# Optimization experiments

Hardware: AMD Instinct MI355X
Metric: run time of the kernel (lower is better)

## Reference

```python
import jax, jax.numpy as jnp
import numpy as np

B, S, D = 2, 2048, 2560
H, HD = 32, 80           # n_head, head_dim = n_embd // n_head
RD = 32                  # rotary_dim (partial rotary, phi-style)
ROPE_BASE = 10000.0


def _rope_cache(seqlen, rotary_dim):
    # inv_freq = 1 / base^(2i/d); freqs = outer(t, inv_freq)  -> [S, RD//2]
    inv_freq = 1.0 / (ROPE_BASE ** (jnp.arange(0, rotary_dim, 2, dtype=jnp.float32) / rotary_dim))
    t = jnp.arange(seqlen, dtype=jnp.float32)
    freqs = jnp.outer(t, inv_freq)
    return jnp.cos(freqs), jnp.sin(freqs)


def setup_inputs() -> dict:
    key = jax.random.key(0)
    k0, k1, k2, k3, k4 = jax.random.split(key, 5)
    x = jax.random.normal(k0, (B, S, D), dtype=jnp.float32)
    wqkv_w = jax.random.normal(k1, (3 * D, D), dtype=jnp.float32) * 0.02
    wqkv_b = jax.random.normal(k2, (3 * D,), dtype=jnp.float32) * 0.02
    out_w = jax.random.normal(k3, (D, D), dtype=jnp.float32) * 0.02
    out_b = jax.random.normal(k4, (D,), dtype=jnp.float32) * 0.02
    return {"x": x, "wqkv_w": wqkv_w, "wqkv_b": wqkv_b, "out_w": out_w, "out_b": out_b}


def _attention_core(x, wqkv_w, wqkv_b, out_w, out_b):
    b, s, d = x.shape
    qkv = (x @ wqkv_w.T + wqkv_b).reshape(b, s, 3, H, HD)  # [B,S,3,H,HD]

    cos, sin = _rope_cache(s, RD)            # [S, RD//2]
    c = cos[:, None, :]                       # [S,1,RD//2]
    si = sin[:, None, :]

    def rot(t):  # partial NeoX-style rotary on first RD dims; t: [B,S,H,HD]
        t_rot, t_pass = t[..., :RD], t[..., RD:]
        t1, t2 = t_rot[..., : RD // 2], t_rot[..., RD // 2 :]
        return jnp.concatenate([t1 * c - t2 * si, t1 * si + t2 * c, t_pass], axis=-1)

    q = rot(qkv[:, :, 0])                     # [B,S,H,HD]
    k = rot(qkv[:, :, 1])
    v = qkv[:, :, 2]

    # fp32 scores = q @ (k * scale)^T, causal mask filled with -10000.0 (as in source)
    scale = 1.0 / np.sqrt(HD).astype(np.float32)
    scores = jnp.einsum("bqhd,bkhd->bhqk", q, k * scale)  # [B,H,S,S]
    causal_mask = jnp.arange(s)[None, :] > jnp.arange(s)[:, None]  # cols > rows
    scores = jnp.where(causal_mask, jnp.float32(-10000.0), scores)
    attn = jax.nn.softmax(scores, axis=-1)
    ctx = jnp.einsum("bhqk,bkhd->bqhd", attn, v).reshape(b, s, d)
    return ctx @ out_w.T + out_b


def reference(x, wqkv_w, wqkv_b, out_w, out_b):
    return _attention_core(x, wqkv_w, wqkv_b, out_w, out_b)
```

## Files before the change

### kernel.cpp

```cpp
#include <hip/hip_runtime.h>
#include <cstdint>
#include <cstddef>

#define B_  2
#define S_  2048
#define D_  2560
#define H_  32
#define HD_ 80

typedef __attribute__((ext_vector_type(8))) short  short8;
typedef __attribute__((ext_vector_type(4))) float  floatx4;

__device__ __forceinline__ float b2f(unsigned short u) {
  union { unsigned int i; float f; } x; x.i = ((unsigned int)u) << 16; return x.f;
}
__device__ __forceinline__ unsigned short f2bf(float f) {
  union { float f; unsigned int i; } x; x.f = f;
  unsigned int u = x.i;
  return (unsigned short)((u + 0x7fffu + ((u >> 16) & 1u)) >> 16);
}

__global__ void cvt3_kernel(const float* __restrict__ s0, unsigned short* __restrict__ d0, int n0,
                            const float* __restrict__ s1, unsigned short* __restrict__ d1, int n1,
                            const float* __restrict__ s2, unsigned short* __restrict__ d2, int n2) {
  int j = blockIdx.x * 256 + threadIdx.x;
  const float* s; unsigned short* d;
  if (j < n0) { s = s0; d = d0; }
  else {
    j -= n0;
    if (j < n1) { s = s1; d = d1; }
    else { j -= n1; if (j >= n2) return; s = s2; d = d2; }
  }
  const float4 v = ((const float4*)s)[j];
  ushort4 r;
  r.x = f2bf(v.x); r.y = f2bf(v.y); r.z = f2bf(v.z); r.w = f2bf(v.w);
  ((ushort4*)d)[j] = r;
}

#define GLOAD_LDS16(g, l)                                                      \
  __builtin_amdgcn_global_load_lds(                                            \
      (const __attribute__((address_space(1))) void*)(g),                      \
      (__attribute__((address_space(3))) void*)(l), 16, 0, 0)

template <int OUT_BF16, int MSUB, int NSUB>
__global__ __launch_bounds__(512)
void gemm256(const unsigned short* __restrict__ A,
             const unsigned short* __restrict__ Bw,
             const float* __restrict__ bias,
             void* __restrict__ Cv,
             const int M, const int N, const int K) {
  constexpr int ASH  = MSUB * 2048;
  constexpr int BSH  = NSUB * 4096;
  constexpr int CBUF = ASH + BSH;
  __shared__ __align__(16) unsigned short sh[2 * CBUF];
  const int tid  = threadIdx.x;
  const int wave = tid >> 6;
  const int lane = tid & 63;
  const int wm = wave >> 2;
  const int wn = wave & 3;
  const int fr = lane & 15;
  const int fg = lane >> 4;
  const int row0 = (int)blockIdx.y * (MSUB * 32);
  const int col0 = (int)blockIdx.x * (NSUB * 64);
  const unsigned short* Ab = A  + (size_t)row0 * K;
  const unsigned short* Bb = Bw + (size_t)col0 * K;
  const int srow = lane >> 2;
  const int scol = ((lane & 3) << 3) ^ ((lane & 32) ? 16 : 0);
  const int rdoff = fr * 32 + ((fg * 8) ^ ((fr & 8) ? 16 : 0));
  const int aOff = wm * (MSUB == 8 ? 8192 : 2048);
  const int bOff = ASH + (NSUB == 4 ? (wn >> 1) * 8192 : 0);
  const int rbB  = (NSUB == 4 ? (wn & 1) * 4 : wn * 2);
  const int NT = K >> 6;

  floatx4 acc[MSUB][NSUB] = {};

#define STAGE_HALF(G, matOff, c, h, k0)                                        \
  do {                                                                         \
    _Pragma("unroll")                                                          \
    for (int i_ = 0; i_ < 2; ++i_) {                                           \
      const int s_ = (wave << 1) | i_;                                         \
      const int kk_ = s_ >> 3, rb_ = s_ & 7;                                   \
      GLOAD_LDS16((G) + (size_t)((h) * 128 + rb_ * 16 + srow) * K              \
                      + ((k0) + kk_ * 32 + scol),                              \
                  &sh[(c) * CBUF + (matOff) + (h) * 8192 + s_ * 512]);         \
    }                                                                          \
  } while (0)

  STAGE_HALF(Ab, 0, 0, 0, 0);
  if (MSUB == 8) STAGE_HALF(Ab, 0, 0, 1, 0);
  STAGE_HALF(Bb, ASH, 0, 0, 0);
  if (NSUB == 4) STAGE_HALF(Bb, ASH, 0, 1, 0);
  asm volatile("s_waitcnt vmcnt(0)" ::: "memory");
  __builtin_amdgcn_s_barrier();

  for (int t = 0; t < NT; ++t) {
    const int c  = t & 1;
    const int cb = c * CBUF;
    if (t + 1 < NT) {
      const int k1 = (t + 1) << 6;
      STAGE_HALF(Ab, 0, c ^ 1, 0, k1);
      if (MSUB == 8) STAGE_HALF(Ab, 0, c ^ 1, 1, k1);
      STAGE_HALF(Bb, ASH, c ^ 1, 0, k1);
      if (NSUB == 4) STAGE_HALF(Bb, ASH, c ^ 1, 1, k1);
    }
    short8 aL[4][2], aH[4][2], bF0[2][2], bF1[2][2];
#pragma unroll
    for (int nj = 0; nj < 2; ++nj)
#pragma unroll
      for (int kk = 0; kk < 2; ++kk)
        bF0[nj][kk] = *(const short8*)&sh[cb + bOff + (kk * 8 + rbB + nj) * 512 + rdoff];
#pragma unroll
    for (int mi = 0; mi < 4; ++mi)
#pragma unroll
      for (int kk = 0; kk < 2; ++kk)
        aL[mi][kk] = *(const short8*)&sh[cb + aOff + (kk * 8 + mi) * 512 + rdoff];
    if (NSUB == 4) {
#pragma unroll
      for (int nj = 0; nj < 2; ++nj)
#pragma unroll
        for (int kk = 0; kk < 2; ++kk)
          bF1[nj][kk] = *(const short8*)&sh[cb + bOff + (kk * 8 + rbB + 2 + nj) * 512 + rdoff];
    }
    __builtin_amdgcn_s_setprio(1);
#pragma unroll
    for (int kk = 0; kk < 2; ++kk)
#pragma unroll
      for (int mi = 0; mi < 4; ++mi)
#pragma unroll
        for (int nj = 0; nj < 2; ++nj)
          acc[mi][nj] = __builtin_amdgcn_mfma_f32_16x16x32_bf16(aL[mi][kk], bF0[nj][kk], acc[mi][nj], 0, 0, 0);
    __builtin_amdgcn_s_setprio(0);
    if (MSUB == 8) {
#pragma unroll
      for (int mi = 0; mi < 4; ++mi)
#pragma unroll
        for (int kk = 0; kk < 2; ++kk)
          aH[mi][kk] = *(const short8*)&sh[cb + aOff + (kk * 8 + 4 + mi) * 512 + rdoff];
    }
    __builtin_amdgcn_s_setprio(1);
    if (NSUB == 4) {
#pragma unroll
      for (int kk = 0; kk < 2; ++kk)
#pragma unroll
        for (int mi = 0; mi < 4; ++mi)
#pragma unroll
          for (int nj = 0; nj < 2; ++nj)
            acc[mi][2 + nj] = __builtin_amdgcn_mfma_f32_16x16x32_bf16(aL[mi][kk], bF1[nj][kk], acc[mi][2 + nj], 0, 0, 0);
      if (MSUB == 8) {
#pragma unroll
        for (int kk = 0; kk < 2; ++kk)
#pragma unroll
          for (int mi = 0; mi < 4; ++mi)
#pragma unroll
            for (int nj = 0; nj < 2; ++nj)
              acc[4 + mi][2 + nj] = __builtin_amdgcn_mfma_f32_16x16x32_bf16(aH[mi][kk], bF1[nj][kk], acc[4 + mi][2 + nj], 0, 0, 0);
      }
    }
    if (MSUB == 8) {
#pragma unroll
      for (int kk = 0; kk < 2; ++kk)
#pragma unroll
        for (int mi = 0; mi < 4; ++mi)
#pragma unroll
          for (int nj = 0; nj < 2; ++nj)
            acc[4 + mi][nj] = __builtin_amdgcn_mfma_f32_16x16x32_bf16(aH[mi][kk], bF0[nj][kk], acc[4 + mi][nj], 0, 0, 0);
    }
    __builtin_amdgcn_s_setprio(0);
    if (t + 1 < NT) {
      asm volatile("s_waitcnt vmcnt(0)" ::: "memory");
      __builtin_amdgcn_s_barrier();
    }
  }
#undef STAGE_HALF

  unsigned short* Cb = (unsigned short*)Cv;
  float* Cf = (float*)Cv;
#pragma unroll
  for (int nj = 0; nj < NSUB; ++nj) {
    const int col = col0 + wn * (NSUB == 4 ? 64 : 32) + nj * 16 + fr;
    const float bv = bias[col];
#pragma unroll
    for (int mi = 0; mi < MSUB; ++mi) {
      const int rowb = row0 + wm * (MSUB * 16) + mi * 16 + fg * 4;
#pragma unroll
      for (int r = 0; r < 4; ++r) {
        const float v = acc[mi][nj][r] + bv;
        const size_t idx = (size_t)(rowb + r) * N + col;
        if (OUT_BF16) Cb[idx] = f2bf(v);
        else          Cf[idx] = v;
      }
    }
  }
}

__global__ void rope_kernel(const unsigned short* __restrict__ qkv,
                            unsigned short* __restrict__ Q,
                            unsigned short* __restrict__ K) {
  const int idx = blockIdx.x * 256 + threadIdx.x;
  if (idx >= B_ * S_ * H_) return;
  const int h = idx & (H_ - 1);
  const int s = (idx >> 5) & (S_ - 1);
  const int b = idx >> 16;
  const unsigned short* row = qkv + (size_t)(b * S_ + s) * (3 * D_);
  const size_t obase = ((size_t)(b * H_ + h) * S_ + s) * HD_;

  float cc[16], ssn[16];
#pragma unroll
  for (int i = 0; i < 16; i++) {
    const float ang = (float)s * exp2f((float)i * -0.83048202372184059f);
    ssn[i] = sinf(ang);
    cc[i]  = cosf(ang);
  }
  {
    const float QS = 0.11180339887498949f * 1.4426950408889634f;
    const uint4* src = (const uint4*)(row + h * HD_);
    float f[80], g[80];
#pragma unroll
    for (int i = 0; i < 10; i++) {
      uint4 t = src[i];
      const unsigned short* w = (const unsigned short*)&t;
#pragma unroll
      for (int j = 0; j < 8; j++) f[i * 8 + j] = b2f(w[j]);
    }
#pragma unroll
    for (int i = 0; i < 16; i++) {
      g[i]      = f[i] * cc[i] - f[i + 16] * ssn[i];
      g[i + 16] = f[i] * ssn[i] + f[i + 16] * cc[i];
    }
#pragma unroll
    for (int i = 32; i < 80; i++) g[i] = f[i];
    uint4* dst = (uint4*)(Q + obase);
#pragma unroll
    for (int i = 0; i < 10; i++) {
      uint4 t;
      unsigned short* w = (unsigned short*)&t;
#pragma unroll
      for (int j = 0; j < 8; j++) w[j] = f2bf(g[i * 8 + j] * QS);
      dst[i] = t;
    }
  }
  {
    const uint4* src = (const uint4*)(row + (H_ + h) * HD_);
    float f[32], g[32];
#pragma unroll
    for (int i = 0; i < 4; i++) {
      uint4 t = src[i];
      const unsigned short* w = (const unsigned short*)&t;
#pragma unroll
      for (int j = 0; j < 8; j++) f[i * 8 + j] = b2f(w[j]);
    }
#pragma unroll
    for (int i = 0; i < 16; i++) {
      g[i]      = f[i] * cc[i] - f[i + 16] * ssn[i];
      g[i + 16] = f[i] * ssn[i] + f[i + 16] * cc[i];
    }
    uint4* dst = (uint4*)(K + obase);
#pragma unroll
    for (int i = 0; i < 4; i++) {
      uint4 t;
      unsigned short* w = (unsigned short*)&t;
#pragma unroll
      for (int j = 0; j < 8; j++) w[j] = f2bf(g[i * 8 + j]);
      dst[i] = t;
    }
#pragma unroll
    for (int i = 4; i < 10; i++) dst[i] = src[i];
  }
}

__global__ __launch_bounds__(256)
void vtrans_kernel(const unsigned short* __restrict__ qkv, unsigned short* __restrict__ Vt) {
  __shared__ unsigned short T[64][88];
  const int tid = threadIdx.x;
  const int bh = blockIdx.y;
  const int b = bh >> 5, h = bh & 31;
  const int tile = blockIdx.x;
  const int s0 = tile * 64;
  for (int t = tid; t < 640; t += 256) {
    const int r = t / 10, c = t % 10;
    const size_t src = ((size_t)((b * S_ + s0 + r) * 3) + 2) * D_ + h * HD_ + c * 8;
    *(uint4*)&T[r][c * 8] = *(const uint4*)&qkv[src];
  }
  __syncthreads();
  unsigned short* tb = Vt + ((size_t)bh * 32 + tile) * 5120;
  for (int t = tid; t < 640; t += 256) {
    const int d = t / 8, sc = t % 8;
    uint4 o;
    unsigned short* w = (unsigned short*)&o;
#pragma unroll
    for (int j = 0; j < 8; j++) w[j] = T[sc * 8 + j][d];
    *(uint4*)&tb[d * 64 + ((sc * 8) ^ ((d & 7) * 8))] = o;
  }
}

__global__ __launch_bounds__(256, 3)
void attn_mfma(const unsigned short* __restrict__ Qg,
               const unsigned short* __restrict__ Kg,
               const unsigned short* __restrict__ Vtg,
               unsigned short* __restrict__ ctx) {
  __shared__ unsigned short Ks[2][64 * 80];
  __shared__ unsigned short Vs[2][80 * 64];
  __shared__ unsigned short Ts[4][32 * 40];

  const int tid  = threadIdx.x;
  const int wave = tid >> 6;
  const int lane = tid & 63;
  const int fr   = lane & 15;
  const int fg   = lane >> 4;
  int p = (int)(blockIdx.y * gridDim.x + blockIdx.x);
  p = (p & 7) * 128 + (p >> 3);
  const int bh = p >> 4;
  const int qt = 15 - (p & 15);
  const int qbase = (qt << 7) + wave * 32;

  const unsigned short* Qrow  = Qg  + (size_t)bh * S_ * HD_;
  const unsigned short* Krow  = Kg  + (size_t)bh * S_ * HD_;
  const unsigned short* Vtile = Vtg + (size_t)bh * 32 * 5120;

  short8 qf[2][3];
  const short8 zfrag = {};
#pragma unroll
  for (int mi = 0; mi < 2; mi++) {
    const unsigned short* qp = Qrow + (size_t)(qbase + mi * 16 + fr) * HD_;
    qf[mi][0] = *(const short8*)&qp[fg * 8];
    qf[mi][1] = *(const short8*)&qp[32 + fg * 8];
    qf[mi][2] = (fg < 2) ? *(const short8*)&qp[64 + fg * 8] : zfrag;
  }

  floatx4 accOT[5][2] = {};
  float l_part[2] = {0.f, 0.f};

  const int nch = 2 * qt + 2;

#define STAGE_CHUNK(c)                                                         \
  do {                                                                         \
    const int buf_ = (c) & 1;                                                  \
    const unsigned short* Kt_ = Krow + (size_t)(c) * 64 * HD_;                 \
    const unsigned short* Vt_ = Vtile + (size_t)(c) * 5120;                    \
    _Pragma("unroll")                                                          \
    for (int u_ = 0; u_ < 5; ++u_) {                                           \
      const int j_ = wave * 5 + u_;                                            \
      if (j_ < 10) GLOAD_LDS16(Kt_ + j_ * 512 + lane * 8, &Ks[buf_][j_ * 512]);\
      else GLOAD_LDS16(Vt_ + (j_ - 10) * 512 + lane * 8,                       \
                       &Vs[buf_][(j_ - 10) * 512]);                            \
    }                                                                          \
  } while (0)

  STAGE_CHUNK(0);

  for (int c = 0; c < nch; c++) {
    const int k0 = c * 64;
    const int buf = c & 1;
    asm volatile("s_waitcnt vmcnt(0)" ::: "memory");
    __builtin_amdgcn_s_barrier();
    if (c + 1 < nch) STAGE_CHUNK(c + 1);

    floatx4 accST[4][2] = {};
#pragma unroll
    for (int ni = 0; ni < 4; ni++) {
      const unsigned short* kp = &Ks[buf][(ni * 16 + fr) * 80];
      const short8 kf0 = *(const short8*)&kp[fg * 8];
      const short8 kf1 = *(const short8*)&kp[32 + fg * 8];
      const short8 kf2 = *(const short8*)&kp[64 + (fg & 1) * 8];
      accST[ni][0] = __builtin_amdgcn_mfma_f32_16x16x32_bf16(kf0, qf[0][0], accST[ni][0], 0, 0, 0);
      accST[ni][1] = __builtin_amdgcn_mfma_f32_16x16x32_bf16(kf0, qf[1][0], accST[ni][1], 0, 0, 0);
      accST[ni][0] = __builtin_amdgcn_mfma_f32_16x16x32_bf16(kf1, qf[0][1], accST[ni][0], 0, 0, 0);
      accST[ni][1] = __builtin_amdgcn_mfma_f32_16x16x32_bf16(kf1, qf[1][1], accST[ni][1], 0, 0, 0);
      accST[ni][0] = __builtin_amdgcn_mfma_f32_16x16x32_bf16(kf2, qf[0][2], accST[ni][0], 0, 0, 0);
      accST[ni][1] = __builtin_amdgcn_mfma_f32_16x16x32_bf16(kf2, qf[1][2], accST[ni][1], 0, 0, 0);
    }

    if (k0 + 63 > qbase) {
#pragma unroll
      for (int ni = 0; ni < 4; ni++)
#pragma unroll
        for (int mi = 0; mi < 2; mi++) {
          const int qg = qbase + mi * 16 + fr;
#pragma unroll
          for (int r = 0; r < 4; r++) {
            const int kg = k0 + ni * 16 + fg * 4 + r;
            if (kg > qg) accST[ni][mi][r] = -1e30f;
          }
        }
    }

#pragma unroll
    for (int hh = 0; hh < 2; hh++) {
#pragma unroll
      for (int nh = 0; nh < 2; nh++) {
        const int ni = hh * 2 + nh;
#pragma unroll
        for (int mi = 0; mi < 2; mi++) {
          const float p0 = __builtin_amdgcn_exp2f(accST[ni][mi][0]);
          const float p1 = __builtin_amdgcn_exp2f(accST[ni][mi][1]);
          const float p2 = __builtin_amdgcn_exp2f(accST[ni][mi][2]);
          const float p3 = __builtin_amdgcn_exp2f(accST[ni][mi][3]);
          l_part[mi] += (p0 + p1) + (p2 + p3);
          uint2 w;
          w.x = (unsigned)f2bf(p0) | ((unsigned)f2bf(p1) << 16);
          w.y = (unsigned)f2bf(p2) | ((unsigned)f2bf(p3) << 16);
          *(uint2*)&Ts[wave][(mi * 16 + fr) * 40 + nh * 16 + fg * 4] = w;
        }
      }
      const short8 pf0 = *(const short8*)&Ts[wave][fr * 40 + fg * 8];
      const short8 pf1 = *(const short8*)&Ts[wave][(16 + fr) * 40 + fg * 8];
      const int vcol = hh * 32 + fg * 8;
#pragma unroll
      for (int dt = 0; dt < 5; dt++) {
        const short8 vf = *(const short8*)&Vs[buf][(dt * 16 + fr) * 64 + (vcol ^ ((fr & 7) * 8))];
        accOT[dt][0] = __builtin_amdgcn_mfma_f32_16x16x32_bf16(vf, pf0, accOT[dt][0], 0, 0, 0);
        accOT[dt][1] = __builtin_amdgcn_mfma_f32_16x16x32_bf16(vf, pf1, accOT[dt][1], 0, 0, 0);
      }
    }
  }
#undef STAGE_CHUNK

  const int b = bh >> 5, h2 = bh & 31;
#pragma unroll
  for (int mi = 0; mi < 2; mi++) {
    float s = l_part[mi];
    s += __shfl_xor(s, 16);
    s += __shfl_xor(s, 32);
    const float inv = 1.f / s;
    const size_t rowoff = (size_t)(b * S_ + qbase + mi * 16 + fr) * D_ + h2 * HD_;
#pragma unroll
    for (int dt = 0; dt < 5; dt++) {
      const float v0 = accOT[dt][mi][0] * inv;
      const float v1 = accOT[dt][mi][1] * inv;
      const float v2 = accOT[dt][mi][2] * inv;
      const float v3 = accOT[dt][mi][3] * inv;
      uint2 w;
      w.x = (unsigned)f2bf(v0) | ((unsigned)f2bf(v1) << 16);
      w.y = (unsigned)f2bf(v2) | ((unsigned)f2bf(v3) << 16);
      *(uint2*)&ctx[rowoff + dt * 16 + fg * 4] = w;
    }
  }
}

extern "C" void kernel_launch(void* const* d_in, const int* in_sizes, int n_in,
                              void* d_out, int out_size, void* d_ws, size_t ws_size,
                              hipStream_t stream) {
  (void)in_sizes; (void)n_in; (void)out_size; (void)ws_size;
  const float* x      = (const float*)d_in[0];
  const float* wqkv_w = (const float*)d_in[1];
  const float* wqkv_b = (const float*)d_in[2];
  const float* out_w  = (const float*)d_in[3];
  const float* out_b  = (const float*)d_in[4];
  char* ws = (char*)d_ws;

  unsigned short* Xb    = (unsigned short*)(ws + 0);
  unsigned short* Wqkvb = (unsigned short*)(ws + 20971520);
  unsigned short* qkv   = (unsigned short*)(ws + 60293120);
  unsigned short* Qb    = (unsigned short*)(ws + 123207680);
  unsigned short* Kb    = (unsigned short*)(ws + 144179200);
  unsigned short* Woutb = (unsigned short*)(ws + 165150720);
  unsigned short* ctx   = Xb;
  unsigned short* Vtile = (unsigned short*)(ws + 34078720);

  cvt3_kernel<<<35840, 256, 0, stream>>>(x, Xb, 2621440,
                                         wqkv_w, Wqkvb, 4915200,
                                         out_w, Woutb, 1638400);
  gemm256<1, 8, 4><<<dim3(30, 16), 512, 0, stream>>>(Xb, Wqkvb, wqkv_b, (void*)qkv, 4096, 7680, 2560);
  rope_kernel<<<512, 256, 0, stream>>>(qkv, Qb, Kb);
  vtrans_kernel<<<dim3(32, 64), 256, 0, stream>>>(qkv, Vtile);
  attn_mfma<<<dim3(16, 64), 256, 0, stream>>>(Qb, Kb, Vtile, ctx);
  gemm256<0, 8, 2><<<dim3(20, 16), 512, 0, stream>>>(ctx, Woutb, out_b, d_out, 4096, 2560, 2560);
}
```

Before: 562.1 us.

## Use 256-row query tiles with 8 waves in attention and interleave score/PV per half

The attention kernel now runs 512-thread blocks that each cover 256 query rows instead of 128. Each staged K/V chunk is therefore shared by twice as many waves, halving global K/V traffic per query. The score computation is split into two halves, each immediately masked, exponentiated and fed to the PV MFMAs, which lowers peak accumulator register pressure. The output GEMM also switches to a wider tile configuration with half the grid columns. The trade-off is fewer, larger blocks, which worsens causal load imbalance, and a barrier that must now synchronise more waves.

```diff
diff --git a/kernel.cpp b/kernel.cpp
--- a/kernel.cpp
+++ b/kernel.cpp
@@ -293,14 +293,14 @@
   }
 }
 
-__global__ __launch_bounds__(256, 3)
+__global__ __launch_bounds__(512, 4)
 void attn_mfma(const unsigned short* __restrict__ Qg,
                const unsigned short* __restrict__ Kg,
                const unsigned short* __restrict__ Vtg,
                unsigned short* __restrict__ ctx) {
   __shared__ unsigned short Ks[2][64 * 80];
   __shared__ unsigned short Vs[2][80 * 64];
-  __shared__ unsigned short Ts[4][32 * 40];
+  __shared__ unsigned short Ts[8][32 * 40];
 
   const int tid  = threadIdx.x;
   const int wave = tid >> 6;
@@ -308,10 +308,10 @@
   const int fr   = lane & 15;
   const int fg   = lane >> 4;
   int p = (int)(blockIdx.y * gridDim.x + blockIdx.x);
-  p = (p & 7) * 128 + (p >> 3);
-  const int bh = p >> 4;
-  const int qt = 15 - (p & 15);
-  const int qbase = (qt << 7) + wave * 32;
+  p = (p & 7) * 64 + (p >> 3);
+  const int bh = p >> 3;
+  const int qt = 7 - (p & 7);
+  const int qbase = (qt << 8) + wave * 32;
 
   const unsigned short* Qrow  = Qg  + (size_t)bh * S_ * HD_;
   const unsigned short* Krow  = Kg  + (size_t)bh * S_ * HD_;
@@ -330,7 +330,7 @@
   floatx4 accOT[5][2] = {};
   float l_part[2] = {0.f, 0.f};
 
-  const int nch = 2 * qt + 2;
+  const int nch = 4 * qt + 4;
 
 #define STAGE_CHUNK(c)                                                         \
   do {                                                                         \
@@ -338,11 +338,12 @@
     const unsigned short* Kt_ = Krow + (size_t)(c) * 64 * HD_;                 \
     const unsigned short* Vt_ = Vtile + (size_t)(c) * 5120;                    \
     _Pragma("unroll")                                                          \
-    for (int u_ = 0; u_ < 5; ++u_) {                                           \
-      const int j_ = wave * 5 + u_;                                            \
-      if (j_ < 10) GLOAD_LDS16(Kt_ + j_ * 512 + lane * 8, &Ks[buf_][j_ * 512]);\
-      else GLOAD_LDS16(Vt_ + (j_ - 10) * 512 + lane * 8,                       \
-                       &Vs[buf_][(j_ - 10) * 512]);                            \
+    for (int u_ = 0; u_ < 3; ++u_) {                                           \
+      const int j_ = u_ * 8 + wave;                                            \
+      if (j_ < 10)      GLOAD_LDS16(Kt_ + j_ * 512 + lane * 8,                 \
+                                    &Ks[buf_][j_ * 512]);                      \
+      else if (j_ < 20) GLOAD_LDS16(Vt_ + (j_ - 10) * 512 + lane * 8,          \
+                                    &Vs[buf_][(j_ - 10) * 512]);               \
     }                                                                          \
   } while (0)
 
@@ -354,54 +355,52 @@
     asm volatile("s_waitcnt vmcnt(0)" ::: "memory");
     __builtin_amdgcn_s_barrier();
     if (c + 1 < nch) STAGE_CHUNK(c + 1);
-
-    floatx4 accST[4][2] = {};
-#pragma unroll
-    for (int ni = 0; ni < 4; ni++) {
-      const unsigned short* kp = &Ks[buf][(ni * 16 + fr) * 80];
-      const short8 kf0 = *(const short8*)&kp[fg * 8];
-      const short8 kf1 = *(const short8*)&kp[32 + fg * 8];
-      const short8 kf2 = *(const short8*)&kp[64 + (fg & 1) * 8];
-      accST[ni][0] = __builtin_amdgcn_mfma_f32_16x16x32_bf16(kf0, qf[0][0], accST[ni][0], 0, 0, 0);
-      accST[ni][1] = __builtin_amdgcn_mfma_f32_16x16x32_bf16(kf0, qf[1][0], accST[ni][1], 0, 0, 0);
-      accST[ni][0] = __builtin_amdgcn_mfma_f32_16x16x32_bf16(kf1, qf[0][1], accST[ni][0], 0, 0, 0);
-      accST[ni][1] = __builtin_amdgcn_mfma_f32_16x16x32_bf16(kf1, qf[1][1], accST[ni][1], 0, 0, 0);
-      accST[ni][0] = __builtin_amdgcn_mfma_f32_16x16x32_bf16(kf2, qf[0][2], accST[ni][0], 0, 0, 0);
-      accST[ni][1] = __builtin_amdgcn_mfma_f32_16x16x32_bf16(kf2, qf[1][2], accST[ni][1], 0, 0, 0);
-    }
-
-    if (k0 + 63 > qbase) {
-#pragma unroll
-      for (int ni = 0; ni < 4; ni++)
+    const bool diag = (k0 + 63 > qbase);
+
+#pragma unroll
+    for (int hh = 0; hh < 2; hh++) {
+      floatx4 accST[2][2] = {};
+#pragma unroll
+      for (int nl = 0; nl < 2; nl++) {
+        const int ni = hh * 2 + nl;
+        const unsigned short* kp = &Ks[buf][(ni * 16 + fr) * 80];
+        const short8 kf0 = *(const short8*)&kp[fg * 8];
+        const short8 kf1 = *(const short8*)&kp[32 + fg * 8];
+        const short8 kf2 = *(const short8*)&kp[64 + (fg & 1) * 8];
+        accST[nl][0] = __builtin_amdgcn_mfma_f32_16x16x32_bf16(kf0, qf[0][0], accST[nl][0], 0, 0, 0);
+        accST[nl][1] = __builtin_amdgcn_mfma_f32_16x16x32_bf16(kf0, qf[1][0], accST[nl][1], 0, 0, 0);
+        accST[nl][0] = __builtin_amdgcn_mfma_f32_16x16x32_bf16(kf1, qf[0][1], accST[nl][0], 0, 0, 0);
+        accST[nl][1] = __builtin_amdgcn_mfma_f32_16x16x32_bf16(kf1, qf[1][1], accST[nl][1], 0, 0, 0);
+        accST[nl][0] = __builtin_amdgcn_mfma_f32_16x16x32_bf16(kf2, qf[0][2], accST[nl][0], 0, 0, 0);
+        accST[nl][1] = __builtin_amdgcn_mfma_f32_16x16x32_bf16(kf2, qf[1][2], accST[nl][1], 0, 0, 0);
+      }
+      if (diag) {
+#pragma unroll
+        for (int nl = 0; nl < 2; nl++)
+#pragma unroll
+          for (int mi = 0; mi < 2; mi++) {
+            const int qg = qbase + mi * 16 + fr;
+#pragma unroll
+            for (int r = 0; r < 4; r++) {
+              const int kg = k0 + (hh * 2 + nl) * 16 + fg * 4 + r;
+              if (kg > qg) accST[nl][mi][r] = -1e30f;
+            }
+          }
+      }
+#pragma unroll
+      for (int nl = 0; nl < 2; nl++)
 #pragma unroll
         for (int mi = 0; mi < 2; mi++) {
-          const int qg = qbase + mi * 16 + fr;
-#pragma unroll
-          for (int r = 0; r < 4; r++) {
-            const int kg = k0 + ni * 16 + fg * 4 + r;
-            if (kg > qg) accST[ni][mi][r] = -1e30f;
-          }
-        }
-    }
-
-#pragma unroll
-    for (int hh = 0; hh < 2; hh++) {
-#pragma unroll
-      for (int nh = 0; nh < 2; nh++) {
-        const int ni = hh * 2 + nh;
-#pragma unroll
-        for (int mi = 0; mi < 2; mi++) {
-          const float p0 = __builtin_amdgcn_exp2f(accST[ni][mi][0]);
-          const float p1 = __builtin_amdgcn_exp2f(accST[ni][mi][1]);
-          const float p2 = __builtin_amdgcn_exp2f(accST[ni][mi][2]);
-          const float p3 = __builtin_amdgcn_exp2f(accST[ni][mi][3]);
+          const float p0 = __builtin_amdgcn_exp2f(accST[nl][mi][0]);
+          const float p1 = __builtin_amdgcn_exp2f(accST[nl][mi][1]);
+          const float p2 = __builtin_amdgcn_exp2f(accST[nl][mi][2]);
+          const float p3 = __builtin_amdgcn_exp2f(accST[nl][mi][3]);
           l_part[mi] += (p0 + p1) + (p2 + p3);
           uint2 w;
           w.x = (unsigned)f2bf(p0) | ((unsigned)f2bf(p1) << 16);
           w.y = (unsigned)f2bf(p2) | ((unsigned)f2bf(p3) << 16);
-          *(uint2*)&Ts[wave][(mi * 16 + fr) * 40 + nh * 16 + fg * 4] = w;
+          *(uint2*)&Ts[wave][(mi * 16 + fr) * 40 + nl * 16 + fg * 4] = w;
         }
-      }
       const short8 pf0 = *(const short8*)&Ts[wave][fr * 40 + fg * 8];
       const short8 pf1 = *(const short8*)&Ts[wave][(16 + fr) * 40 + fg * 8];
       const int vcol = hh * 32 + fg * 8;
@@ -463,6 +462,6 @@
   gemm256<1, 8, 4><<<dim3(30, 16), 512, 0, stream>>>(Xb, Wqkvb, wqkv_b, (void*)qkv, 4096, 7680, 2560);
   rope_kernel<<<512, 256, 0, stream>>>(qkv, Qb, Kb);
   vtrans_kernel<<<dim3(32, 64), 256, 0, stream>>>(qkv, Vtile);
-  attn_mfma<<<dim3(16, 64), 256, 0, stream>>>(Qb, Kb, Vtile, ctx);
-  gemm256<0, 8, 2><<<dim3(20, 16), 512, 0, stream>>>(ctx, Woutb, out_b, d_out, 4096, 2560, 2560);
-}
+  attn_mfma<<<dim3(8, 64), 512, 0, stream>>>(Qb, Kb, Vtile, ctx);
+  gemm256<0, 8, 4><<<dim3(10, 16), 512, 0, stream>>>(ctx, Woutb, out_b, d_out, 4096, 2560, 2560);
+}
```

New measurement: 558.3 us. No clear change (-0.7%).
